# Kernel optimization log

Measured on AMD Instinct MI355X. Metric: run time of the kernel, lower is better.

## Reference

```python
import jax, jax.numpy as jnp
import numpy as np

H = 1024        # hidden_size
V = 32000       # vocab size (src and tgt)
S = 64          # encoder length == max_length
T = 64          # decoder length
BOS_ID = 0


def setup_inputs() -> dict:
    key = jax.random.key(0)
    ks = jax.random.split(key, 24)
    sc = 0.02
    f = lambda k, shape: (sc * jax.random.normal(k, shape)).astype(jnp.float32)
    inp = {
        "src_tokens": jax.random.randint(ks[0], (S,), 0, V),
        "tgt_tokens": jax.random.randint(ks[1], (T,), 0, V - 1),
        "teacher_forcing_ratio": jnp.float32(1.0),
        # encoder
        "enc_emb": f(ks[2], (V, H)),
        "enc_Wih": f(ks[3], (4 * H, H)),
        "enc_Whh": f(ks[4], (4 * H, H)),
        "enc_bih": f(ks[5], (4 * H,)),
        "enc_bhh": f(ks[6], (4 * H,)),
        # decoder
        "dec_emb": f(ks[7], (V, H)),
        "att_We": f(ks[8], (H, H)),
        "att_be": f(ks[9], (H,)),
        "att_Wu": f(ks[10], (H, H)),
        "att_bu": f(ks[11], (H,)),
        "att_v": f(ks[12], (H,)),
        "w1_W": f(ks[13], (H, 2 * H)),
        "w1_b": f(ks[14], (H,)),
        "w2_W": f(ks[15], (H, 2 * H)),
        "w2_b": f(ks[16], (H,)),
        "dec_Wih": f(ks[17], (4 * H, H)),
        "dec_Whh": f(ks[18], (4 * H, H)),
        "dec_bih": f(ks[19], (4 * H,)),
        "dec_bhh": f(ks[20], (4 * H,)),
        "out_W": f(ks[21], (V, H)),
        "out_b": f(ks[22], (V,)),
    }
    return inp


def _lstm_cell(x, h, c, Wih, Whh, bih, bhh):
    # torch gate order: i, f, g, o
    gates = Wih @ x + bih + Whh @ h + bhh          # [4H]
    i, fg, g, o = jnp.split(gates, 4)
    c2 = jax.nn.sigmoid(fg) * c + jax.nn.sigmoid(i) * jnp.tanh(g)
    h2 = jax.nn.sigmoid(o) * jnp.tanh(c2)
    return h2, c2


def reference(src_tokens, tgt_tokens, teacher_forcing_ratio,
              enc_emb, enc_Wih, enc_Whh, enc_bih, enc_bhh,
              dec_emb, att_We, att_be, att_Wu, att_bu, att_v,
              w1_W, w1_b, w2_W, w2_b,
              dec_Wih, dec_Whh, dec_bih, dec_bhh, out_W, out_b):
    # ---- encoder: single-layer LSTM, batch=1, one token per step ----
    def enc_step(carry, tok):
        h, c = carry
        x = enc_emb[tok]                           # [H]
        h2, c2 = _lstm_cell(x, h, c, enc_Wih, enc_Whh, enc_bih, enc_bhh)
        return (h2, c2), h2

    z = jnp.zeros((H,), enc_emb.dtype)
    (h_enc, c_enc), enc_outs = jax.lax.scan(enc_step, (z, z), src_tokens)  # enc_outs: [S,H]

    # u_decoder(encoder_outputs) is loop-invariant: compute once.
    enc_proj = enc_outs @ att_Wu.T + att_bu        # [S,H]

    # teacher_forcing_ratio = 1.0 -> decoder inputs are [BOS] + target[:-1]
    dec_inputs = jnp.concatenate([jnp.array([BOS_ID], dtype=tgt_tokens.dtype), tgt_tokens[:-1]])

    def dec_step(carry, tok):
        h, c = carry
        x = dec_emb[tok]                            # [H]
        # additive attention: v^T tanh(W_e h + U_d enc_outs)
        combine = att_We @ h + att_be + enc_proj    # [S,H]
        energy = jnp.tanh(combine) @ att_v          # [S]
        w = jax.nn.softmax(energy)                  # [S]
        context = w @ enc_outs                      # [H]
        inp = w1_W @ jnp.concatenate([context, x]) + w1_b   # [H]
        h2, c2 = _lstm_cell(inp, h, c, dec_Wih, dec_Whh, dec_bih, dec_bhh)
        # single-layer LSTM: output == new hidden state h2
        pre = w2_W @ jnp.concatenate([h2, h2]) + w2_b       # [H]
        logits = out_W @ pre + out_b                        # [V]
        return (h2, c2), logits

    _, logits = jax.lax.scan(dec_step, (h_enc, c_enc), dec_inputs)  # [T,V]
    return logits[:, None, :]                       # [T,1,V], matches torch.stack of [1,V]
```

## Files before the change

kernel.cpp:

```cpp
#include <hip/hip_runtime.h>

#define HD 1024
#define VOC 32000
#define SL 64
#define TL 64
#define NWG 256
#define BLK 256

#define SENT 0x7FC0DEADu

#define OFF_HCH    4096
#define OFF_EPT    139264
#define OFF_WIHX   204800
#define OFF_PE     OFF_WIHX
#define OFF_Q      466944
#define OFF_M1     729088
#define OFF_M2     794624
#define OFF_PRET   1056768
#define OFF_XENC   1122304
#define OFF_XDEC   1187840
#define OFF_PRE1   1253376

struct KArgs {
  const int* src; const int* tgt;
  const void *enc_emb, *enc_Wih, *enc_Whh, *enc_bih, *enc_bhh;
  const void *dec_emb, *att_We, *att_be, *att_Wu, *att_bu, *att_v;
  const void *w1_W, *w1_b, *w2_W, *w2_b;
  const void *dec_Wih, *dec_Whh, *dec_bih, *dec_bhh;
  const void *out_W, *out_b;
  void* out; float* ws;
};

__device__ __forceinline__ float bf2f(unsigned short u) {
  unsigned w = ((unsigned)u) << 16; float f; __builtin_memcpy(&f, &w, 4); return f;
}
__device__ __forceinline__ unsigned short f2bf(float f) {
  unsigned u; __builtin_memcpy(&u, &f, 4);
  unsigned r = u + 0x7FFFu + ((u >> 16) & 1u);
  return (unsigned short)(r >> 16);
}
__device__ __forceinline__ float sigmf(float x) { return 1.f / (1.f + expf(-x)); }

__device__ __forceinline__ float ldw(const float* p) {
  return __hip_atomic_load(p, __ATOMIC_RELAXED, __HIP_MEMORY_SCOPE_AGENT);
}
__device__ __forceinline__ void stw(float* p, float v) {
  __hip_atomic_store(p, v, __ATOMIC_RELAXED, __HIP_MEMORY_SCOPE_AGENT);
}
__device__ __forceinline__ unsigned ldu(const unsigned* p) {
  return __hip_atomic_load(p, __ATOMIC_RELAXED, __HIP_MEMORY_SCOPE_AGENT);
}
__device__ __forceinline__ void stu(unsigned* p, unsigned v) {
  __hip_atomic_store(p, v, __ATOMIC_RELAXED, __HIP_MEMORY_SCOPE_AGENT);
}

struct BFT {}; struct FPT {};
template<class DT> struct LD;
template<> struct LD<FPT> {
  static __device__ __forceinline__ float get(const void* p, long i) { return ((const float*)p)[i]; }
};
template<> struct LD<BFT> {
  static __device__ __forceinline__ float get(const void* p, long i) { return bf2f(((const unsigned short*)p)[i]); }
};
template<class DT> struct LD4;
template<> struct LD4<FPT> {
  static __device__ __forceinline__ float4 get(const void* p, long i) {
    return *(const float4*)((const float*)p + i);
  }
};
template<> struct LD4<BFT> {
  static __device__ __forceinline__ float4 get(const void* p, long i) {
    ushort4 u = *(const ushort4*)((const unsigned short*)p + i);
    float4 f; f.x = bf2f(u.x); f.y = bf2f(u.y); f.z = bf2f(u.z); f.w = bf2f(u.w); return f;
  }
};
template<class DT> struct ST;
template<> struct ST<FPT> {
  static __device__ __forceinline__ void put(void* p, long i, float v) { ((float*)p)[i] = v; }
};
template<> struct ST<BFT> {
  static __device__ __forceinline__ void put(void* p, long i, float v) { ((unsigned short*)p)[i] = f2bf(v); }
};

__device__ __forceinline__ void gbar(unsigned* ws_u, unsigned* ep, int tid, int wg) {
  __syncthreads();
  if (tid == 0) {
    unsigned e = ++(*ep);
    unsigned old = __hip_atomic_fetch_add(&ws_u[8 + (wg >> 5)], 1u,
                                          __ATOMIC_RELAXED, __HIP_MEMORY_SCOPE_AGENT);
    if (old == e * 32u - 1u) {
      unsigned o2 = __hip_atomic_fetch_add(&ws_u[16], 1u,
                                           __ATOMIC_RELAXED, __HIP_MEMORY_SCOPE_AGENT);
      if (o2 == e * 8u - 1u) {
        __hip_atomic_store(&ws_u[20], e, __ATOMIC_RELAXED, __HIP_MEMORY_SCOPE_AGENT);
      }
    }
    while (__hip_atomic_load(&ws_u[20], __ATOMIC_RELAXED, __HIP_MEMORY_SCOPE_AGENT) < e) {
      __builtin_amdgcn_s_sleep(2);
    }
  }
  __syncthreads();
}

template<class DT, int NR, bool DUAL, bool TRO>
__device__ void gemm_rows(const void* W, int wstride, int woff, int woff2,
                          int r0, const float* X, float* out, int ostride,
                          const void* b1, const void* b2, int tid, float* s_stage) {
  const int PER = NR / 4;
  float acc[PER];
#pragma unroll
  for (int i = 0; i < PER; ++i) acc[i] = 0.f;
  for (int k0 = 0; k0 < HD; k0 += 128) {
    __syncthreads();
    for (int i = tid; i < 64 * 128; i += BLK) {
      int t = i >> 7, kk = i & 127;
      s_stage[t * 129 + kk] = ldw(&X[t * HD + k0 + kk]);
    }
    __syncthreads();
#pragma unroll
    for (int i = 0; i < PER; ++i) {
      int oi = tid + i * BLK;
      int t = oi & 63, r_l = oi >> 6;
      long r = r0 + r_l;
      long wb = r * wstride + woff + k0;
      long wb2 = r * wstride + woff2 + k0;
      float a = 0.f;
#pragma unroll 8
      for (int kk = 0; kk < 128; kk += 4) {
        float4 wv = LD4<DT>::get(W, wb + kk);
        if (DUAL) {
          float4 w2 = LD4<DT>::get(W, wb2 + kk);
          wv.x += w2.x; wv.y += w2.y; wv.z += w2.z; wv.w += w2.w;
        }
        a += wv.x * s_stage[t * 129 + kk]     + wv.y * s_stage[t * 129 + kk + 1]
           + wv.z * s_stage[t * 129 + kk + 2] + wv.w * s_stage[t * 129 + kk + 3];
      }
      acc[i] += a;
    }
  }
  __syncthreads();
#pragma unroll
  for (int i = 0; i < PER; ++i) {
    int oi = tid + i * BLK;
    int t = oi & 63, r_l = oi >> 6;
    int r = r0 + r_l;
    float v = acc[i];
    if (b1) v += LD<DT>::get(b1, r);
    if (b2) v += LD<DT>::get(b2, r);
    if (TRO) stw(&out[r * ostride + t], v); else stw(&out[t * ostride + r], v);
  }
}

template<class DT>
__device__ void run_all(const KArgs& A, int tid, int wg,
                        float* s_big, float* s_red, float* s_w, float* s_m2,
                        float* s_h, float* s_whh, float* s_wh, float* s_gate, float* s_c,
                        float* s_wx, float* s_q, float* s_ep, float* s_av) {
  float* ws = A.ws;
  unsigned* ws_u = (unsigned*)ws;
  unsigned epoch = 0;
  float* hch   = ws + OFF_HCH;
  float* epT   = ws + OFF_EPT;
  float* WihX  = ws + OFF_WIHX;
  float* peC   = ws + OFF_PE;
  float* Q     = ws + OFF_Q;
  float* M1    = ws + OFF_M1;
  float* M2T   = ws + OFF_M2;
  float* PreT  = ws + OFF_PRET;
  float* Xenc  = ws + OFF_XENC;
  float* Xdec  = ws + OFF_XDEC;
  float* pre1  = ws + OFF_PRE1;
  const int j0 = wg * 4;

  if (tid < 4) s_c[tid] = 0.f;
  {
    unsigned* hu = (unsigned*)hch;
    for (int i = wg * BLK + tid; i < 129 * 1024; i += NWG * BLK) stu(hu + i, SENT);
  }
  if (wg < 64) {
    int t = wg, tok = A.src[t];
    for (int k = tid; k < HD; k += BLK) stw(&Xenc[t * HD + k], LD<DT>::get(A.enc_emb, (long)tok * HD + k));
  } else if (wg < 128) {
    int t = wg - 64;
    int tok = (t == 0) ? 0 : A.tgt[t - 1];
    for (int k = tid; k < HD; k += BLK) stw(&Xdec[t * HD + k], LD<DT>::get(A.dec_emb, (long)tok * HD + k));
  }
  gbar(ws_u, &epoch, tid, wg);

  gemm_rows<DT, 16, false, false>(A.enc_Wih, 1024, 0, 0, wg * 16, Xenc, WihX, 4096,
                                  A.enc_bih, A.enc_bhh, tid, s_big);
  gemm_rows<DT, 4, false, false>(A.w1_W, 2048, 1024, 0, wg * 4, Xdec, pre1, 1024,
                                 A.w1_b, nullptr, tid, s_big);
  gbar(ws_u, &epoch, tid, wg);

  for (int i = tid; i < 1024; i += BLK) {
    int t = i >> 4, l = i & 15;
    s_wx[i] = ldw(&WihX[t * 4096 + ((l >> 2) << 10) + j0 + (l & 3)]);
  }

  const int row_l = tid >> 4, lane = tid & 15;
  const int gg_ = row_l >> 2, qq_ = row_l & 3;
  const int myrow = gg_ * 1024 + j0 + qq_;
  for (int t = 0; t < SL; ++t) {
    if (t == 0) {
      for (int i = tid; i < HD; i += BLK) s_h[i] = 0.f;
    } else {
      const unsigned* hb = (const unsigned*)(hch + (size_t)t * HD);
      unsigned uu[4];
#pragma unroll
      for (int j = 0; j < 4; ++j) uu[j] = ldu(hb + tid + j * BLK);
#pragma unroll
      for (int j = 0; j < 4; ++j) {
        while (uu[j] == SENT) { __builtin_amdgcn_s_sleep(1); uu[j] = ldu(hb + tid + j * BLK); }
        float f; __builtin_memcpy(&f, &uu[j], 4);
        s_h[tid + j * BLK] = f;
      }
    }
    __syncthreads();
    float part = 0.f;
#pragma unroll 4
    for (int j = 0; j < 16; ++j) {
      int k = (lane << 2) + (j << 6);
      float4 wv = LD4<DT>::get(A.enc_Whh, (long)myrow * HD + k);
      const float4 hv = *(const float4*)(s_h + k);
      part += wv.x * hv.x + wv.y * hv.y + wv.z * hv.z + wv.w * hv.w;
    }
    s_red[tid] = part;
    __syncthreads();
    if (tid < 16) {
      float v = 0.f;
      for (int i = 0; i < 16; ++i) v += s_red[tid * 16 + i];
      s_gate[tid] = v + s_wx[t * 16 + tid];
    }
    __syncthreads();
    if (tid < 4) {
      float ig = s_gate[tid], fg = s_gate[4 + tid], gv = s_gate[8 + tid], og = s_gate[12 + tid];
      float c2 = sigmf(fg) * s_c[tid] + sigmf(ig) * tanhf(gv);
      float h2v = sigmf(og) * tanhf(c2);
      s_c[tid] = c2;
      stw(&hch[(size_t)(t + 1) * HD + j0 + tid], h2v);
    }
  }

  gemm_rows<DT, 4, false, true>(A.att_Wu, 1024, 0, 0, wg * 4, hch + HD, epT, 64,
                                A.att_bu, nullptr, tid, s_big);
  gemm_rows<DT, 4, false, false>(A.w1_W, 2048, 0, 0, wg * 4, hch + HD, M1, 1024,
                                 nullptr, nullptr, tid, s_big);
  {
    unsigned* pu = (unsigned*)peC;
    for (int i = tid; i < 1024; i += BLK) stu(pu + wg * 1024 + i, SENT);
  }
  gbar(ws_u, &epoch, tid, wg);

  gemm_rows<DT, 16, false, false>(A.dec_Wih, 1024, 0, 0, wg * 16, M1, M2T, 4096,
                                  nullptr, nullptr, tid, s_big);
  gemm_rows<DT, 16, false, false>(A.dec_Wih, 1024, 0, 0, wg * 16, pre1, Q, 4096,
                                  A.dec_bih, A.dec_bhh, tid, s_big);
  gbar(ws_u, &epoch, tid, wg);

  for (int i = tid; i < 1024; i += BLK) {
    int l = i >> 6, s = i & 63;
    s_m2[l * 65 + s] = ldw(&M2T[s * 4096 + ((l >> 2) << 10) + j0 + (l & 3)]);
  }
  for (int i = tid; i < 1024; i += BLK) {
    int t = i >> 4, l = i & 15;
    s_q[i] = ldw(&Q[t * 4096 + ((l >> 2) << 10) + j0 + (l & 3)]);
  }
  if (wg < 64) {
    for (int i = tid; i < 1024; i += BLK) s_ep[i] = ldw(&epT[wg * 1024 + i]);
    if (tid < 16) s_av[tid] = LD<DT>::get(A.att_v, wg * 16 + tid);
  }

  for (int t = 0; t < TL; ++t) {
    {
      const unsigned* hb = (const unsigned*)(hch + (size_t)(64 + t) * HD);
      unsigned uu[4];
#pragma unroll
      for (int j = 0; j < 4; ++j) uu[j] = ldu(hb + tid + j * BLK);
#pragma unroll
      for (int j = 0; j < 4; ++j) {
        while (uu[j] == SENT) { __builtin_amdgcn_s_sleep(1); uu[j] = ldu(hb + tid + j * BLK); }
        float f; __builtin_memcpy(&f, &uu[j], 4);
        s_h[tid + j * BLK] = f;
      }
    }
    __syncthreads();
    if (wg < 64) {
      float p2 = 0.f;
#pragma unroll 4
      for (int j = 0; j < 16; ++j) {
        int k = (lane << 2) + (j << 6);
        float4 wv = LD4<DT>::get(A.att_We, (long)(wg * 16 + row_l) * HD + k);
        const float4 hv = *(const float4*)(s_h + k);
        p2 += wv.x * hv.x + wv.y * hv.y + wv.z * hv.z + wv.w * hv.w;
      }
      s_red[tid] = p2;
      __syncthreads();
      if (tid < 16) {
        float v2 = 0.f;
        for (int i = 0; i < 16; ++i) v2 += s_red[tid * 16 + i];
        s_wh[tid] = v2 + LD<DT>::get(A.att_be, wg * 16 + tid);
      }
      __syncthreads();
      if (tid < 64) {
        float pe = 0.f;
#pragma unroll
        for (int jj = 0; jj < 16; ++jj)
          pe += s_av[jj] * tanhf(s_wh[jj] + s_ep[jj * 64 + tid]);
        stw(&peC[(size_t)t * 4096 + wg * 64 + tid], pe);
      }
    }
    float part = 0.f;
#pragma unroll 4
    for (int j = 0; j < 16; ++j) {
      int k = (lane << 2) + (j << 6);
      float4 wv = LD4<DT>::get(A.dec_Whh, (long)myrow * HD + k);
      const float4 hv = *(const float4*)(s_h + k);
      part += wv.x * hv.x + wv.y * hv.y + wv.z * hv.z + wv.w * hv.w;
    }
    s_red[tid] = part;
    __syncthreads();
    if (tid < 16) {
      float v = 0.f;
      for (int i = 0; i < 16; ++i) v += s_red[tid * 16 + i];
      s_whh[tid] = v;
    }
    __syncthreads();
    {
      int s = tid & 63, gb = tid >> 6;
      const unsigned* pb = (const unsigned*)(peC + (size_t)t * 4096) + s;
      unsigned uu[16];
#pragma unroll
      for (int j = 0; j < 16; ++j) uu[j] = ldu(pb + (gb * 16 + j) * 64);
      float pe = 0.f;
#pragma unroll
      for (int j = 0; j < 16; ++j) {
        while (uu[j] == SENT) { __builtin_amdgcn_s_sleep(1); uu[j] = ldu(pb + (gb * 16 + j) * 64); }
        float f; __builtin_memcpy(&f, &uu[j], 4); pe += f;
      }
      s_red[tid] = pe;
    }
    __syncthreads();
    if (tid < 64) {
      float x = s_red[tid] + s_red[64 + tid] + s_red[128 + tid] + s_red[192 + tid];
      float m = x;
#pragma unroll
      for (int d = 32; d >= 1; d >>= 1) m = fmaxf(m, __shfl_xor(m, d, 64));
      float e = expf(x - m);
      float su = e;
#pragma unroll
      for (int d = 32; d >= 1; d >>= 1) su += __shfl_xor(su, d, 64);
      s_w[tid] = e;
      if (tid == 0) s_w[64] = 1.f / su;
    }
    __syncthreads();
    if (tid < 16) {
      float ctx = 0.f;
#pragma unroll 8
      for (int s2 = 0; s2 < 64; ++s2) ctx += s_m2[tid * 65 + s2] * s_w[s2];
      s_gate[tid] = s_whh[tid] + s_q[t * 16 + tid] + ctx * s_w[64];
    }
    __syncthreads();
    if (tid < 4) {
      float ig = s_gate[tid], fg = s_gate[4 + tid], gv = s_gate[8 + tid], og = s_gate[12 + tid];
      float c2 = sigmf(fg) * s_c[tid] + sigmf(ig) * tanhf(gv);
      float h2v = sigmf(og) * tanhf(c2);
      s_c[tid] = c2;
      stw(&hch[(size_t)(65 + t) * HD + j0 + tid], h2v);
    }
  }

  gemm_rows<DT, 4, true, true>(A.w2_W, 2048, 0, 1024, wg * 4, hch + 65 * HD, PreT, 64,
                               A.w2_b, nullptr, tid, s_big);
  gbar(ws_u, &epoch, tid, wg);

  {
    const int t = tid & 63, kq = tid >> 6;
    const int v0 = wg * 125;
    for (int vg = 0; vg < 5; ++vg) {
      float acc[25];
#pragma unroll
      for (int i = 0; i < 25; ++i) acc[i] = 0.f;
      for (int kc = 0; kc < 8; ++kc) {
        __syncthreads();
        for (int i = tid; i < 128 * 64; i += BLK) {
          int kk = i >> 6, tt = i & 63;
          s_big[kk * 66 + tt] = ldw(&PreT[(kc * 128 + kk) * 64 + tt]);
        }
        __syncthreads();
        float p[32];
#pragma unroll
        for (int k = 0; k < 32; ++k) p[k] = s_big[(kq * 32 + k) * 66 + t];
        for (int i = 0; i < 25; ++i) {
          int v = v0 + vg * 25 + i;
          long wb = (long)v * HD + kc * 128 + kq * 32;
          float a = 0.f;
#pragma unroll
          for (int k = 0; k < 32; k += 4) {
            float4 wv = LD4<DT>::get(A.out_W, wb + k);
            a += wv.x * p[k] + wv.y * p[k + 1] + wv.z * p[k + 2] + wv.w * p[k + 3];
          }
          acc[i] += a;
        }
      }
      __syncthreads();
#pragma unroll
      for (int i = 0; i < 25; ++i) s_big[i * 256 + tid] = acc[i];
      __syncthreads();
      for (int o = tid; o < 1600; o += BLK) {
        int tt = o / 25, i = o - tt * 25;
        int v = v0 + vg * 25 + i;
        float r2 = s_big[i * 256 + tt] + s_big[i * 256 + 64 + tt] + s_big[i * 256 + 128 + tt]
                 + s_big[i * 256 + 192 + tt] + LD<DT>::get(A.out_b, v);
        ST<DT>::put(A.out, (long)tt * VOC + v, r2);
      }
      __syncthreads();
    }
  }
}

__global__ __launch_bounds__(BLK)
void lstm_seq2seq_kernel(KArgs A) {
  __shared__ __align__(16) float s_big[8448];
  __shared__ float s_red[BLK];
  __shared__ float s_w[66];
  __shared__ float s_m2[16 * 65];
  __shared__ __align__(16) float s_h[HD];
  __shared__ float s_whh[16];
  __shared__ float s_wh[16];
  __shared__ float s_gate[16];
  __shared__ float s_c[4];
  __shared__ float s_wx[1024];
  __shared__ float s_q[1024];
  __shared__ float s_ep[1024];
  __shared__ float s_av[16];
  __shared__ int s_flag;

  const int tid = threadIdx.x, wg = blockIdx.x;

  {
    const unsigned* pw = (const unsigned*)A.enc_Wih;
    int hits = 0;
    for (int i = tid; i < 4096; i += BLK) {
      unsigned ex = (pw[i] >> 7) & 0xFFu;
      hits += (ex >= 100u && ex <= 126u) ? 1 : 0;
    }
    s_red[tid] = (float)hits;
    __syncthreads();
    for (int s = BLK / 2; s > 0; s >>= 1) {
      if (tid < s) s_red[tid] += s_red[tid + s];
      __syncthreads();
    }
    if (tid == 0) s_flag = (s_red[0] > 2048.0f) ? 1 : 0;
    __syncthreads();
  }

  if (s_flag) run_all<BFT>(A, tid, wg, s_big, s_red, s_w, s_m2, s_h, s_whh, s_wh, s_gate, s_c,
                           s_wx, s_q, s_ep, s_av);
  else        run_all<FPT>(A, tid, wg, s_big, s_red, s_w, s_m2, s_h, s_whh, s_wh, s_gate, s_c,
                           s_wx, s_q, s_ep, s_av);
}

extern "C" void kernel_launch(void* const* d_in, const int* in_sizes, int n_in,
                              void* d_out, int out_size, void* d_ws, size_t ws_size,
                              hipStream_t stream) {
  (void)in_sizes; (void)n_in; (void)out_size; (void)ws_size;
  hipMemsetAsync(d_ws, 0, 256, stream);
  KArgs a;
  a.src = (const int*)d_in[0];
  a.tgt = (const int*)d_in[1];
  a.enc_emb = d_in[3]; a.enc_Wih = d_in[4]; a.enc_Whh = d_in[5];
  a.enc_bih = d_in[6]; a.enc_bhh = d_in[7];
  a.dec_emb = d_in[8]; a.att_We = d_in[9]; a.att_be = d_in[10];
  a.att_Wu = d_in[11]; a.att_bu = d_in[12]; a.att_v = d_in[13];
  a.w1_W = d_in[14]; a.w1_b = d_in[15]; a.w2_W = d_in[16]; a.w2_b = d_in[17];
  a.dec_Wih = d_in[18]; a.dec_Whh = d_in[19]; a.dec_bih = d_in[20]; a.dec_bhh = d_in[21];
  a.out_W = d_in[22]; a.out_b = d_in[23];
  a.out = d_out; a.ws = (float*)d_ws;
  hipLaunchKernelGGL(lstm_seq2seq_kernel, dim3(NWG), dim3(BLK), 0, stream, a);
}
```

Before: 2.481 ms.

## Cache recurrent weights in registers and shorten per-step sync in LSTM loops

Loads the encoder Whh rows and the attention We rows into registers once, before the time loops, instead of re-reading them from memory every step. Replaces the shared-memory row reductions with wave shuffles, which removes barriers per step. Polling is now a sweep over all words at once, and the attention-partials loads are issued before the decoder Whh dot product so they overlap. The context reduction is spread across 64 threads, and explicit polls wait for the final hidden state after each loop. This raises register pressure and may lower occupancy or cause spills.

```diff
diff --git a/kernel.cpp b/kernel.cpp
--- a/kernel.cpp
+++ b/kernel.cpp
@@ -52,6 +52,21 @@
 }
 __device__ __forceinline__ void stu(unsigned* p, unsigned v) {
   __hip_atomic_store(p, v, __ATOMIC_RELAXED, __HIP_MEMORY_SCOPE_AGENT);
+}
+
+template<int N>
+__device__ __forceinline__ void sweep_poll(const unsigned* base, int stride, unsigned* uu) {
+#pragma unroll
+  for (int j = 0; j < N; ++j) uu[j] = ldu(base + j * stride);
+  for (;;) {
+    bool need = false;
+#pragma unroll
+    for (int j = 0; j < N; ++j) need |= (uu[j] == SENT);
+    if (!need) return;
+    __builtin_amdgcn_s_sleep(1);
+#pragma unroll
+    for (int j = 0; j < N; ++j) uu[j] = ldu(base + j * stride);
+  }
 }
 
 struct BFT {}; struct FPT {};
@@ -201,45 +216,45 @@
   const int row_l = tid >> 4, lane = tid & 15;
   const int gg_ = row_l >> 2, qq_ = row_l & 3;
   const int myrow = gg_ * 1024 + j0 + qq_;
+
+  float4 wrec[16];
+#pragma unroll
+  for (int j = 0; j < 16; ++j)
+    wrec[j] = LD4<DT>::get(A.enc_Whh, (long)myrow * HD + (lane << 2) + (j << 6));
+
   for (int t = 0; t < SL; ++t) {
     if (t == 0) {
       for (int i = tid; i < HD; i += BLK) s_h[i] = 0.f;
     } else {
       const unsigned* hb = (const unsigned*)(hch + (size_t)t * HD);
       unsigned uu[4];
-#pragma unroll
-      for (int j = 0; j < 4; ++j) uu[j] = ldu(hb + tid + j * BLK);
-#pragma unroll
-      for (int j = 0; j < 4; ++j) {
-        while (uu[j] == SENT) { __builtin_amdgcn_s_sleep(1); uu[j] = ldu(hb + tid + j * BLK); }
-        float f; __builtin_memcpy(&f, &uu[j], 4);
-        s_h[tid + j * BLK] = f;
-      }
+      sweep_poll<4>(hb + tid, BLK, uu);
+#pragma unroll
+      for (int j = 0; j < 4; ++j) { float f; __builtin_memcpy(&f, &uu[j], 4); s_h[tid + j * BLK] = f; }
     }
     __syncthreads();
     float part = 0.f;
-#pragma unroll 4
+#pragma unroll
     for (int j = 0; j < 16; ++j) {
-      int k = (lane << 2) + (j << 6);
-      float4 wv = LD4<DT>::get(A.enc_Whh, (long)myrow * HD + k);
-      const float4 hv = *(const float4*)(s_h + k);
-      part += wv.x * hv.x + wv.y * hv.y + wv.z * hv.z + wv.w * hv.w;
-    }
-    s_red[tid] = part;
-    __syncthreads();
-    if (tid < 16) {
-      float v = 0.f;
-      for (int i = 0; i < 16; ++i) v += s_red[tid * 16 + i];
-      s_gate[tid] = v + s_wx[t * 16 + tid];
-    }
+      const float4 hv = *(const float4*)(s_h + (lane << 2) + (j << 6));
+      part += wrec[j].x * hv.x + wrec[j].y * hv.y + wrec[j].z * hv.z + wrec[j].w * hv.w;
+    }
+#pragma unroll
+    for (int d = 8; d >= 1; d >>= 1) part += __shfl_xor(part, d, 64);
+    if ((tid & 15) == 0) s_red[row_l] = part + s_wx[t * 16 + row_l];
     __syncthreads();
     if (tid < 4) {
-      float ig = s_gate[tid], fg = s_gate[4 + tid], gv = s_gate[8 + tid], og = s_gate[12 + tid];
+      float ig = s_red[tid], fg = s_red[4 + tid], gv = s_red[8 + tid], og = s_red[12 + tid];
       float c2 = sigmf(fg) * s_c[tid] + sigmf(ig) * tanhf(gv);
       float h2v = sigmf(og) * tanhf(c2);
       s_c[tid] = c2;
       stw(&hch[(size_t)(t + 1) * HD + j0 + tid], h2v);
     }
+  }
+
+  {
+    unsigned uu[4];
+    sweep_poll<4>((const unsigned*)(hch + (size_t)64 * HD) + tid, BLK, uu);
   }
 
   gemm_rows<DT, 4, false, true>(A.att_Wu, 1024, 0, 0, wg * 4, hch + HD, epT, 64,
@@ -270,37 +285,32 @@
     for (int i = tid; i < 1024; i += BLK) s_ep[i] = ldw(&epT[wg * 1024 + i]);
     if (tid < 16) s_av[tid] = LD<DT>::get(A.att_v, wg * 16 + tid);
   }
+  float4 wwe[16];
+  if (wg < 64) {
+#pragma unroll
+    for (int j = 0; j < 16; ++j)
+      wwe[j] = LD4<DT>::get(A.att_We, (long)(wg * 16 + row_l) * HD + (lane << 2) + (j << 6));
+  }
 
   for (int t = 0; t < TL; ++t) {
     {
       const unsigned* hb = (const unsigned*)(hch + (size_t)(64 + t) * HD);
       unsigned uu[4];
-#pragma unroll
-      for (int j = 0; j < 4; ++j) uu[j] = ldu(hb + tid + j * BLK);
-#pragma unroll
-      for (int j = 0; j < 4; ++j) {
-        while (uu[j] == SENT) { __builtin_amdgcn_s_sleep(1); uu[j] = ldu(hb + tid + j * BLK); }
-        float f; __builtin_memcpy(&f, &uu[j], 4);
-        s_h[tid + j * BLK] = f;
-      }
+      sweep_poll<4>(hb + tid, BLK, uu);
+#pragma unroll
+      for (int j = 0; j < 4; ++j) { float f; __builtin_memcpy(&f, &uu[j], 4); s_h[tid + j * BLK] = f; }
     }
     __syncthreads();
     if (wg < 64) {
       float p2 = 0.f;
-#pragma unroll 4
+#pragma unroll
       for (int j = 0; j < 16; ++j) {
-        int k = (lane << 2) + (j << 6);
-        float4 wv = LD4<DT>::get(A.att_We, (long)(wg * 16 + row_l) * HD + k);
-        const float4 hv = *(const float4*)(s_h + k);
-        p2 += wv.x * hv.x + wv.y * hv.y + wv.z * hv.z + wv.w * hv.w;
-      }
-      s_red[tid] = p2;
-      __syncthreads();
-      if (tid < 16) {
-        float v2 = 0.f;
-        for (int i = 0; i < 16; ++i) v2 += s_red[tid * 16 + i];
-        s_wh[tid] = v2 + LD<DT>::get(A.att_be, wg * 16 + tid);
-      }
+        const float4 hv = *(const float4*)(s_h + (lane << 2) + (j << 6));
+        p2 += wwe[j].x * hv.x + wwe[j].y * hv.y + wwe[j].z * hv.z + wwe[j].w * hv.w;
+      }
+#pragma unroll
+      for (int d = 8; d >= 1; d >>= 1) p2 += __shfl_xor(p2, d, 64);
+      if ((tid & 15) == 0) s_wh[row_l] = p2 + LD<DT>::get(A.att_be, wg * 16 + row_l);
       __syncthreads();
       if (tid < 64) {
         float pe = 0.f;
@@ -310,36 +320,35 @@
         stw(&peC[(size_t)t * 4096 + wg * 64 + tid], pe);
       }
     }
+    const int s_ = tid & 63, gb = tid >> 6;
+    const unsigned* pb = (const unsigned*)(peC + (size_t)t * 4096) + s_;
+    unsigned uu[16];
+#pragma unroll
+    for (int j = 0; j < 16; ++j) uu[j] = ldu(pb + (gb * 16 + j) * 64);
     float part = 0.f;
-#pragma unroll 4
+#pragma unroll
     for (int j = 0; j < 16; ++j) {
       int k = (lane << 2) + (j << 6);
       float4 wv = LD4<DT>::get(A.dec_Whh, (long)myrow * HD + k);
       const float4 hv = *(const float4*)(s_h + k);
       part += wv.x * hv.x + wv.y * hv.y + wv.z * hv.z + wv.w * hv.w;
     }
-    s_red[tid] = part;
-    __syncthreads();
-    if (tid < 16) {
-      float v = 0.f;
-      for (int i = 0; i < 16; ++i) v += s_red[tid * 16 + i];
-      s_whh[tid] = v;
-    }
-    __syncthreads();
-    {
-      int s = tid & 63, gb = tid >> 6;
-      const unsigned* pb = (const unsigned*)(peC + (size_t)t * 4096) + s;
-      unsigned uu[16];
+#pragma unroll
+    for (int d = 8; d >= 1; d >>= 1) part += __shfl_xor(part, d, 64);
+    if ((tid & 15) == 0) s_whh[row_l] = part;
+    for (;;) {
+      bool need = false;
+#pragma unroll
+      for (int j = 0; j < 16; ++j) need |= (uu[j] == SENT);
+      if (!need) break;
+      __builtin_amdgcn_s_sleep(1);
 #pragma unroll
       for (int j = 0; j < 16; ++j) uu[j] = ldu(pb + (gb * 16 + j) * 64);
-      float pe = 0.f;
-#pragma unroll
-      for (int j = 0; j < 16; ++j) {
-        while (uu[j] == SENT) { __builtin_amdgcn_s_sleep(1); uu[j] = ldu(pb + (gb * 16 + j) * 64); }
-        float f; __builtin_memcpy(&f, &uu[j], 4); pe += f;
-      }
-      s_red[tid] = pe;
-    }
+    }
+    float pe = 0.f;
+#pragma unroll
+    for (int j = 0; j < 16; ++j) { float f; __builtin_memcpy(&f, &uu[j], 4); pe += f; }
+    s_red[tid] = pe;
     __syncthreads();
     if (tid < 64) {
       float x = s_red[tid] + s_red[64 + tid] + s_red[128 + tid] + s_red[192 + tid];
@@ -354,12 +363,15 @@
       if (tid == 0) s_w[64] = 1.f / su;
     }
     __syncthreads();
-    if (tid < 16) {
-      float ctx = 0.f;
-#pragma unroll 8
-      for (int s2 = 0; s2 < 64; ++s2) ctx += s_m2[tid * 65 + s2] * s_w[s2];
-      s_gate[tid] = s_whh[tid] + s_q[t * 16 + tid] + ctx * s_w[64];
-    }
+    float ctxp = 0.f;
+    if (tid < 64) {
+      int l = tid & 15, g = tid >> 4;
+#pragma unroll
+      for (int s2 = g * 16; s2 < g * 16 + 16; ++s2) ctxp += s_m2[l * 65 + s2] * s_w[s2];
+      ctxp += __shfl_xor(ctxp, 16, 64);
+      ctxp += __shfl_xor(ctxp, 32, 64);
+    }
+    if (tid < 16) s_gate[tid] = s_whh[tid] + s_q[t * 16 + tid] + ctxp * s_w[64];
     __syncthreads();
     if (tid < 4) {
       float ig = s_gate[tid], fg = s_gate[4 + tid], gv = s_gate[8 + tid], og = s_gate[12 + tid];
@@ -368,6 +380,11 @@
       s_c[tid] = c2;
       stw(&hch[(size_t)(65 + t) * HD + j0 + tid], h2v);
     }
+  }
+
+  {
+    unsigned uu[4];
+    sweep_poll<4>((const unsigned*)(hch + (size_t)128 * HD) + tid, BLK, uu);
   }
 
   gemm_rows<DT, 4, true, true>(A.w2_W, 2048, 0, 1024, wg * 4, hch + 65 * HD, PreT, 64,
```

Result: faster. 2.207 ms (-11.1%).
